# Kernel tuning notes

Hardware: AMD Instinct MI355X
Metric: run time of the kernel (lower is better)

Reference implementation:

```python
import jax, jax.numpy as jnp
import numpy as np

B, N, C, H = 8, 2048, 384, 6
D = C // H  # head dim = 64
SCALE = D ** -0.5


def setup_inputs() -> dict:
    key = jax.random.key(0)
    k1, k2, k3, k4 = jax.random.split(key, 4)
    x = jax.random.normal(k1, (B, N, C), dtype=jnp.float32)
    prompt = jnp.zeros((1,), dtype=jnp.float32)  # unused by forward
    mask = jax.random.uniform(k2, (B, N, N), dtype=jnp.float32)
    qkv_w = jax.random.normal(k3, (3 * C, C), dtype=jnp.float32) * (C ** -0.5)
    proj_w = jax.random.normal(k4, (C, C), dtype=jnp.float32) * (C ** -0.5)
    proj_b = jnp.zeros((C,), dtype=jnp.float32)
    return {"x": x, "prompt": prompt, "mask": mask,
            "qkv_w": qkv_w, "proj_w": proj_w, "proj_b": proj_b}


def reference(x, prompt, mask, qkv_w, proj_w, proj_b):
    b, n, c = x.shape
    # qkv: Linear(dim, 3*dim, bias=False) -> (B,N,3,H,D) -> (3,B,H,N,D)
    qkv = (x @ qkv_w.T).reshape(b, n, 3, H, D).transpose(2, 0, 3, 1, 4)
    q, k, v = qkv[0], qkv[1], qkv[2]
    # attn scores with additive mask (mask * -1e5), softmax over keys
    attn = jnp.einsum('bhqd,bhkd->bhqk', q, k) * SCALE
    attn = attn + (mask * -100000.0)[:, None, :, :]
    attn = jax.nn.softmax(attn, axis=-1)
    out = jnp.einsum('bhqk,bhkd->bhqd', attn, v)  # (B,H,N,D)
    out = out.transpose(0, 2, 1, 3).reshape(b, n, c)
    return out @ proj_w.T + proj_b
```

## Files before the change

### kernel.cpp

```cpp
#include <hip/hip_runtime.h>
#include <stdint.h>
#include <math.h>

#define BB 8
#define SEQ 2048
#define CDIM 384
#define NH 6
#define HD 64
#define QKVN 1152

typedef __attribute__((ext_vector_type(8))) __bf16 bf16x8;
typedef __attribute__((ext_vector_type(4))) __bf16 bf16x4;
typedef __attribute__((ext_vector_type(4))) float f32x4;
typedef __attribute__((ext_vector_type(4))) unsigned short ushort4v;

__device__ __forceinline__ unsigned short f2bf(float f) {
  unsigned int u = __float_as_uint(f);
  u += 0x7fffu + ((u >> 16) & 1u);
  return (unsigned short)(u >> 16);
}

__global__ void k_convert(const float* __restrict__ src, unsigned short* __restrict__ dst, int n4) {
  int i = blockIdx.x * blockDim.x + threadIdx.x;
  if (i >= n4) return;
  float4 f = reinterpret_cast<const float4*>(src)[i];
  ushort4v u;
  u.x = f2bf(f.x); u.y = f2bf(f.y); u.z = f2bf(f.z); u.w = f2bf(f.w);
  reinterpret_cast<ushort4v*>(dst)[i] = u;
}

__device__ __forceinline__ void gload_lds16(const unsigned short* g, unsigned short* l) {
  __builtin_amdgcn_global_load_lds((const __attribute__((address_space(1))) void*)g,
                                   (__attribute__((address_space(3))) void*)l, 16, 0, 0);
}

template<int OUT_F32>
__global__ __launch_bounds__(256, 2) void k_gemm_bt(
    const unsigned short* __restrict__ A, const unsigned short* __restrict__ Bm,
    unsigned short* __restrict__ Cb, float* __restrict__ Cf,
    const float* __restrict__ bias, int M, int Nc, int K)
{
  __shared__ unsigned short lA[128 * 32];
  __shared__ unsigned short lB[128 * 32];
  const int t = threadIdx.x;
  const int w = t >> 6, l = t & 63;
  const int wr = w >> 1, wc = w & 1;
  const int row0 = blockIdx.x * 128, col0 = blockIdx.y * 128;
  const f32x4 vzero = {0.f, 0.f, 0.f, 0.f};
  f32x4 acc[4][4];
#pragma unroll
  for (int m = 0; m < 4; ++m)
#pragma unroll
    for (int n = 0; n < 4; ++n) acc[m][n] = vzero;

  const int srow = w * 16 + (l >> 2);
  const int scol = (l & 3) * 8;
  const int lr = l & 15, kc = (l >> 4) * 8;

  for (int k0 = 0; k0 < K; k0 += 32) {
#pragma unroll
    for (int r = 0; r < 2; ++r) {
      gload_lds16(A + (size_t)(row0 + r * 64 + srow) * K + k0 + scol,
                  &lA[(r * 64 + srow) * 32 + scol]);
      gload_lds16(Bm + (size_t)(col0 + r * 64 + srow) * K + k0 + scol,
                  &lB[(r * 64 + srow) * 32 + scol]);
    }
    __syncthreads();
    bf16x8 af[4], bfr[4];
#pragma unroll
    for (int m = 0; m < 4; ++m)
      af[m] = *(const bf16x8*)&lA[(wr * 64 + m * 16 + lr) * 32 + kc];
#pragma unroll
    for (int n = 0; n < 4; ++n)
      bfr[n] = *(const bf16x8*)&lB[(wc * 64 + n * 16 + lr) * 32 + kc];
#pragma unroll
    for (int m = 0; m < 4; ++m)
#pragma unroll
      for (int n = 0; n < 4; ++n)
        acc[m][n] = __builtin_amdgcn_mfma_f32_16x16x32_bf16(af[m], bfr[n], acc[m][n], 0, 0, 0);
    __syncthreads();
  }

#pragma unroll
  for (int m = 0; m < 4; ++m) {
    const int row = row0 + wr * 64 + m * 16 + (l >> 4) * 4;
#pragma unroll
    for (int n = 0; n < 4; ++n) {
      const int col = col0 + wc * 64 + n * 16 + (l & 15);
      if (OUT_F32) {
        const float bv = bias[col];
#pragma unroll
        for (int j = 0; j < 4; ++j)
          Cf[(size_t)(row + j) * Nc + col] = acc[m][n][j] + bv;
      } else {
#pragma unroll
        for (int j = 0; j < 4; ++j)
          Cb[(size_t)(row + j) * Nc + col] = f2bf(acc[m][n][j]);
      }
    }
  }
}

__global__ void k_vtrans(const unsigned short* __restrict__ qkv, unsigned short* __restrict__ vt)
{
  __shared__ unsigned short tile[64][76];
  const int bh = blockIdx.x;
  const int b = bh / NH, h = bh - b * NH;
  const int n0 = blockIdx.y * 64;
  const int t = threadIdx.x;
  const int rr0 = t >> 4;
  const int c4 = (t & 15) * 4;
  const unsigned short* src = qkv + (size_t)(b * SEQ + n0) * QKVN + 2 * CDIM + h * HD;
#pragma unroll
  for (int rr = 0; rr < 4; ++rr) {
    int n = rr * 16 + rr0;
    ushort4v v = *(const ushort4v*)(src + (size_t)n * QKVN + c4);
    *(ushort4v*)&tile[n][c4] = v;
  }
  __syncthreads();
  unsigned short* dst = vt + (size_t)bh * HD * SEQ + n0;
#pragma unroll
  for (int rr = 0; rr < 4; ++rr) {
    int d = rr * 16 + rr0;
    ushort4v v;
    v.x = tile[c4 + 0][d];
    v.y = tile[c4 + 1][d];
    v.z = tile[c4 + 2][d];
    v.w = tile[c4 + 3][d];
    *(ushort4v*)(dst + (size_t)d * SEQ + c4) = v;
  }
}

__global__ __launch_bounds__(256, 4) void k_attn(
    const unsigned short* __restrict__ qkv, const float* __restrict__ mask,
    const unsigned short* __restrict__ vt, unsigned short* __restrict__ aout)
{
  const int bid = blockIdx.x;
  const int b = bid & 7;
  const int g2 = bid >> 3;
  const int h = g2 % NH;
  const int nt = g2 / NH;
  const int t = threadIdx.x;
  const int w = t >> 6, l = t & 63;
  const int gk = l >> 4, c = l & 15;
  const int q0 = nt * 64 + w * 16;

  __shared__ unsigned short lK[2][4096];
  __shared__ unsigned short lV[2][4096];

  const unsigned short* qb = qkv + (size_t)(b * SEQ + q0) * QKVN + h * HD;
  const unsigned short* kb = qkv + (size_t)(b * SEQ) * QKVN + CDIM + h * HD;
  const unsigned short* vb = vt + (size_t)(b * NH + h) * HD * SEQ;
  const float* mrowc = mask + ((size_t)b * SEQ + q0 + c) * SEQ + 4 * gk;

  const int trow = t >> 3, tg = t & 7;
  const int glog = tg ^ (trow & 7);
  const size_t kSrc = (size_t)trow * QKVN + glog * 8;
  const size_t vSrc = (size_t)trow * SEQ + glog * 8;
  const int tid8 = t * 8;

  const int fr0 = c * 64 + ((gk) ^ (c & 7)) * 8;
  const int fr1 = c * 64 + ((4 + gk) ^ (c & 7)) * 8;
  const int cx2 = 2 * (c & 7);
  const int vg0 = c * 64 + ((gk) ^ cx2) * 4;
  const int vg1 = c * 64 + ((4 + gk) ^ cx2) * 4;
  const int vg2 = c * 64 + ((8 + gk) ^ cx2) * 4;
  const int vg3 = c * 64 + ((12 + gk) ^ cx2) * 4;

  bf16x8 qf0 = *(const bf16x8*)(qb + (size_t)c * QKVN + gk * 8);
  bf16x8 qf1 = *(const bf16x8*)(qb + (size_t)c * QKVN + 32 + gk * 8);
#pragma unroll
  for (int i = 0; i < 8; ++i) {
    qf0[i] = (__bf16)((float)qf0[i] * 0.18033688f);
    qf1[i] = (__bf16)((float)qf1[i] * 0.18033688f);
  }

  const f32x4 vzero = {0.f, 0.f, 0.f, 0.f};
  f32x4 acco[4];
  float mreg = -INFINITY, asum = 0.f;
#pragma unroll
  for (int dt = 0; dt < 4; ++dt) acco[dt] = vzero;

#pragma unroll
  for (int j = 0; j < 2; ++j) {
    gload_lds16(kb + (size_t)j * 32 * QKVN + kSrc, &lK[0][j * 2048 + tid8]);
    gload_lds16(vb + (size_t)j * 32 * SEQ + vSrc, &lV[0][j * 2048 + tid8]);
  }
  float4 mk[4];
#pragma unroll
  for (int j = 0; j < 4; ++j)
    mk[j] = *(const float4*)(mrowc + 16 * j);
  int buf = 0;

  for (int kt = 0; kt < SEQ; kt += 64) {
    const bool haveNext = (kt + 64 < SEQ);
    __syncthreads();
    if (haveNext) {
#pragma unroll
      for (int j = 0; j < 2; ++j) {
        gload_lds16(kb + (size_t)(kt + 64 + j * 32) * QKVN + kSrc, &lK[buf ^ 1][j * 2048 + tid8]);
        gload_lds16(vb + (kt + 64) + (size_t)j * 32 * SEQ + vSrc, &lV[buf ^ 1][j * 2048 + tid8]);
      }
    }

    f32x4 s[4];
#pragma unroll
    for (int j = 0; j < 4; ++j) {
      bf16x8 kfa = *(const bf16x8*)&lK[buf][j * 1024 + fr0];
      bf16x8 kfb = *(const bf16x8*)&lK[buf][j * 1024 + fr1];
      s[j] = __builtin_amdgcn_mfma_f32_16x16x32_bf16(kfa, qf0, vzero, 0, 0, 0);
      s[j] = __builtin_amdgcn_mfma_f32_16x16x32_bf16(kfb, qf1, s[j], 0, 0, 0);
    }

#pragma unroll
    for (int j = 0; j < 4; ++j) {
      const float* mkf = (const float*)&mk[j];
#pragma unroll
      for (int r = 0; r < 4; ++r)
        s[j][r] = fmaf(mkf[r], -144269.50f, s[j][r]);
    }
    if (haveNext) {
#pragma unroll
      for (int j = 0; j < 4; ++j)
        mk[j] = *(const float4*)(mrowc + kt + 64 + 16 * j);
    }

    float tm = fmaxf(fmaxf(fmaxf(s[0][0], s[0][1]), fmaxf(s[0][2], s[0][3])),
                     fmaxf(fmaxf(s[1][0], s[1][1]), fmaxf(s[1][2], s[1][3])));
    tm = fmaxf(tm, fmaxf(fmaxf(fmaxf(s[2][0], s[2][1]), fmaxf(s[2][2], s[2][3])),
                         fmaxf(fmaxf(s[3][0], s[3][1]), fmaxf(s[3][2], s[3][3]))));
    tm = fmaxf(tm, __shfl_xor(tm, 16));
    tm = fmaxf(tm, __shfl_xor(tm, 32));

    if (__any(tm > mreg + 8.f)) {
      const float mn = fmaxf(mreg, tm);
      const float al = __builtin_amdgcn_exp2f(mreg - mn);
      mreg = mn;
      asum *= al;
      float alr[4];
#pragma unroll
      for (int r = 0; r < 4; ++r)
        alr[r] = __shfl(al, 20 * gk + r);
#pragma unroll
      for (int dt = 0; dt < 4; ++dt)
#pragma unroll
        for (int r = 0; r < 4; ++r)
          acco[dt][r] *= alr[r];
    }

#pragma unroll
    for (int j = 0; j < 4; ++j)
#pragma unroll
      for (int r = 0; r < 4; ++r)
        s[j][r] = __builtin_amdgcn_exp2f(s[j][r] - mreg);
    float rs = ((s[0][0] + s[0][1]) + (s[0][2] + s[0][3]))
             + ((s[1][0] + s[1][1]) + (s[1][2] + s[1][3]))
             + ((s[2][0] + s[2][1]) + (s[2][2] + s[2][3]))
             + ((s[3][0] + s[3][1]) + (s[3][2] + s[3][3]));
    rs += __shfl_xor(rs, 16);
    rs += __shfl_xor(rs, 32);
    asum += rs;

    union { unsigned int u[8]; bf16x8 v[2]; } pu;
#pragma unroll
    for (int j = 0; j < 4; ++j) {
      asm("v_cvt_pk_bf16_f32 %0, %1, %2" : "=v"(pu.u[2 * j]) : "v"(s[j][0]), "v"(s[j][1]));
      asm("v_cvt_pk_bf16_f32 %0, %1, %2" : "=v"(pu.u[2 * j + 1]) : "v"(s[j][2]), "v"(s[j][3]));
    }
    bf16x8 pf0 = pu.v[0];
    bf16x8 pf1 = pu.v[1];

#pragma unroll
    for (int dt = 0; dt < 4; ++dt) {
      const unsigned short* vrow = &lV[buf][dt * 1024];
      bf16x4 a0 = *(const bf16x4*)(vrow + vg0);
      bf16x4 a1 = *(const bf16x4*)(vrow + vg1);
      bf16x4 a2 = *(const bf16x4*)(vrow + vg2);
      bf16x4 a3 = *(const bf16x4*)(vrow + vg3);
      bf16x8 vf0 = __builtin_shufflevector(a0, a1, 0, 1, 2, 3, 4, 5, 6, 7);
      bf16x8 vf1 = __builtin_shufflevector(a2, a3, 0, 1, 2, 3, 4, 5, 6, 7);
      acco[dt] = __builtin_amdgcn_mfma_f32_16x16x32_bf16(pf0, vf0, acco[dt], 0, 0, 0);
      acco[dt] = __builtin_amdgcn_mfma_f32_16x16x32_bf16(pf1, vf1, acco[dt], 0, 0, 0);
    }
    buf ^= 1;
  }

  float invr[4];
#pragma unroll
  for (int r = 0; r < 4; ++r)
    invr[r] = 1.0f / __shfl(asum, 20 * gk + r);
  unsigned short* ob = aout + (size_t)(b * SEQ + q0) * CDIM + h * HD;
#pragma unroll
  for (int r = 0; r < 4; ++r)
#pragma unroll
    for (int dt = 0; dt < 4; ++dt)
      ob[(size_t)(4 * gk + r) * CDIM + dt * 16 + c] = f2bf(acco[dt][r] * invr[r]);
}

extern "C" void kernel_launch(void* const* d_in, const int* in_sizes, int n_in,
                              void* d_out, int out_size, void* d_ws, size_t ws_size,
                              hipStream_t stream) {
  (void)in_sizes; (void)n_in; (void)out_size; (void)ws_size;
  const float* x      = (const float*)d_in[0];
  const float* mask   = (const float*)d_in[2];
  const float* qkv_w  = (const float*)d_in[3];
  const float* proj_w = (const float*)d_in[4];
  const float* proj_b = (const float*)d_in[5];
  float* out = (float*)d_out;
  char* ws = (char*)d_ws;

  unsigned short* xb    = (unsigned short*)(ws + 0);
  unsigned short* wqb   = (unsigned short*)(ws + 12582912);
  unsigned short* wpb   = (unsigned short*)(ws + 13467648);
  unsigned short* qkvb  = (unsigned short*)(ws + 13762560);
  unsigned short* vtb   = (unsigned short*)(ws + 51511296);
  unsigned short* aoutb = (unsigned short*)(ws + 64094208);

  k_convert<<<6144, 256, 0, stream>>>(x, xb, 1572864);
  k_convert<<<432, 256, 0, stream>>>(qkv_w, wqb, 110592);
  k_convert<<<144, 256, 0, stream>>>(proj_w, wpb, 36864);
  k_gemm_bt<0><<<dim3(128, 9), 256, 0, stream>>>(xb, wqb, qkvb, nullptr, nullptr, 16384, 1152, 384);
  k_vtrans<<<dim3(48, 32), 256, 0, stream>>>(qkvb, vtb);
  k_attn<<<1536, 256, 0, stream>>>(qkvb, mask, vtb, aoutb);
  k_gemm_bt<1><<<dim3(128, 3), 256, 0, stream>>>(aoutb, wpb, nullptr, out, proj_b, 16384, 384, 384);
}
```

Measured before the change: 198.2 us.

## Rework attention kernel to 32x32 MFMA tiles with 32 queries per wave

The attention kernel now has each wave handle 32 query rows using 32x32x16 bf16 MFMAs instead of 16 rows with 16x16x32 MFMAs. This doubles the queries per block, halves the grid, and lets each K/V tile loaded into LDS serve twice as many queries. The softmax row sum is now computed by an extra MFMA against a ones vector, and P is rearranged with permlane32 swaps. It also adds s_setprio around the MFMA sections and loads the mask inside the loop instead of prefetching it. The cost is higher register pressure (launch bounds lowered to 2) and less latency hiding on the mask loads.

```diff
diff --git a/kernel.cpp b/kernel.cpp
--- a/kernel.cpp
+++ b/kernel.cpp
@@ -10,8 +10,8 @@
 #define QKVN 1152
 
 typedef __attribute__((ext_vector_type(8))) __bf16 bf16x8;
-typedef __attribute__((ext_vector_type(4))) __bf16 bf16x4;
 typedef __attribute__((ext_vector_type(4))) float f32x4;
+typedef __attribute__((ext_vector_type(16))) float f32x16;
 typedef __attribute__((ext_vector_type(4))) unsigned short ushort4v;
 
 __device__ __forceinline__ unsigned short f2bf(float f) {
@@ -131,7 +131,7 @@
   }
 }
 
-__global__ __launch_bounds__(256, 4) void k_attn(
+__global__ __launch_bounds__(256, 2) void k_attn(
     const unsigned short* __restrict__ qkv, const float* __restrict__ mask,
     const unsigned short* __restrict__ vt, unsigned short* __restrict__ aout)
 {
@@ -142,16 +142,15 @@
   const int nt = g2 / NH;
   const int t = threadIdx.x;
   const int w = t >> 6, l = t & 63;
-  const int gk = l >> 4, c = l & 15;
-  const int q0 = nt * 64 + w * 16;
+  const int ql = l & 31, hl = l >> 5;
+  const int q0w = nt * 128 + w * 32;
 
   __shared__ unsigned short lK[2][4096];
   __shared__ unsigned short lV[2][4096];
 
-  const unsigned short* qb = qkv + (size_t)(b * SEQ + q0) * QKVN + h * HD;
   const unsigned short* kb = qkv + (size_t)(b * SEQ) * QKVN + CDIM + h * HD;
   const unsigned short* vb = vt + (size_t)(b * NH + h) * HD * SEQ;
-  const float* mrowc = mask + ((size_t)b * SEQ + q0 + c) * SEQ + 4 * gk;
+  const float* mrowq = mask + ((size_t)b * SEQ + q0w + ql) * SEQ + 4 * hl;
 
   const int trow = t >> 3, tg = t & 7;
   const int glog = tg ^ (trow & 7);
@@ -159,37 +158,37 @@
   const size_t vSrc = (size_t)trow * SEQ + glog * 8;
   const int tid8 = t * 8;
 
-  const int fr0 = c * 64 + ((gk) ^ (c & 7)) * 8;
-  const int fr1 = c * 64 + ((4 + gk) ^ (c & 7)) * 8;
-  const int cx2 = 2 * (c & 7);
-  const int vg0 = c * 64 + ((gk) ^ cx2) * 4;
-  const int vg1 = c * 64 + ((4 + gk) ^ cx2) * 4;
-  const int vg2 = c * 64 + ((8 + gk) ^ cx2) * 4;
-  const int vg3 = c * 64 + ((12 + gk) ^ cx2) * 4;
-
-  bf16x8 qf0 = *(const bf16x8*)(qb + (size_t)c * QKVN + gk * 8);
-  bf16x8 qf1 = *(const bf16x8*)(qb + (size_t)c * QKVN + 32 + gk * 8);
-#pragma unroll
-  for (int i = 0; i < 8; ++i) {
-    qf0[i] = (__bf16)((float)qf0[i] * 0.18033688f);
-    qf1[i] = (__bf16)((float)qf1[i] * 0.18033688f);
-  }
-
-  const f32x4 vzero = {0.f, 0.f, 0.f, 0.f};
-  f32x4 acco[4];
-  float mreg = -INFINITY, asum = 0.f;
-#pragma unroll
-  for (int dt = 0; dt < 4; ++dt) acco[dt] = vzero;
+  const int qx = ql & 7;
+  int off0[4], off1[4];
+#pragma unroll
+  for (int i = 0; i < 4; ++i) {
+    const int g = ((2 * i + hl) ^ qx) * 8;
+    off0[i] = ql * 64 + g;
+    off1[i] = (32 + ql) * 64 + g;
+  }
+
+  const unsigned short* qb = qkv + (size_t)(b * SEQ + q0w + ql) * QKVN + h * HD;
+  bf16x8 qf[4];
+#pragma unroll
+  for (int m = 0; m < 4; ++m) {
+    qf[m] = *(const bf16x8*)(qb + 16 * m + 8 * hl);
+#pragma unroll
+    for (int i = 0; i < 8; ++i)
+      qf[m][i] = (__bf16)((float)qf[m][i] * 0.18033688f);
+  }
+
+  const __bf16 one = (__bf16)1.0f;
+  const bf16x8 vones = {one, one, one, one, one, one, one, one};
+  f32x16 acco0, acco1, asum;
+#pragma unroll
+  for (int i = 0; i < 16; ++i) { acco0[i] = 0.f; acco1[i] = 0.f; asum[i] = 0.f; }
+  float mreg = -INFINITY;
 
 #pragma unroll
   for (int j = 0; j < 2; ++j) {
     gload_lds16(kb + (size_t)j * 32 * QKVN + kSrc, &lK[0][j * 2048 + tid8]);
     gload_lds16(vb + (size_t)j * 32 * SEQ + vSrc, &lV[0][j * 2048 + tid8]);
   }
-  float4 mk[4];
-#pragma unroll
-  for (int j = 0; j < 4; ++j)
-    mk[j] = *(const float4*)(mrowc + 16 * j);
   int buf = 0;
 
   for (int kt = 0; kt < SEQ; kt += 64) {
@@ -203,98 +202,101 @@
       }
     }
 
-    f32x4 s[4];
+    float4 mk[8];
+#pragma unroll
+    for (int s = 0; s < 8; ++s)
+      mk[s] = *(const float4*)(mrowq + kt + 8 * s);
+
+    f32x16 s0, s1;
+#pragma unroll
+    for (int i = 0; i < 16; ++i) { s0[i] = 0.f; s1[i] = 0.f; }
+    __builtin_amdgcn_s_setprio(1);
+#pragma unroll
+    for (int m = 0; m < 4; ++m) {
+      bf16x8 kfa = *(const bf16x8*)&lK[buf][off0[m]];
+      bf16x8 kfb = *(const bf16x8*)&lK[buf][off1[m]];
+      s0 = __builtin_amdgcn_mfma_f32_32x32x16_bf16(kfa, qf[m], s0, 0, 0, 0);
+      s1 = __builtin_amdgcn_mfma_f32_32x32x16_bf16(kfb, qf[m], s1, 0, 0, 0);
+    }
+    __builtin_amdgcn_s_setprio(0);
+
 #pragma unroll
     for (int j = 0; j < 4; ++j) {
-      bf16x8 kfa = *(const bf16x8*)&lK[buf][j * 1024 + fr0];
-      bf16x8 kfb = *(const bf16x8*)&lK[buf][j * 1024 + fr1];
-      s[j] = __builtin_amdgcn_mfma_f32_16x16x32_bf16(kfa, qf0, vzero, 0, 0, 0);
-      s[j] = __builtin_amdgcn_mfma_f32_16x16x32_bf16(kfb, qf1, s[j], 0, 0, 0);
-    }
-
-#pragma unroll
-    for (int j = 0; j < 4; ++j) {
-      const float* mkf = (const float*)&mk[j];
-#pragma unroll
-      for (int r = 0; r < 4; ++r)
-        s[j][r] = fmaf(mkf[r], -144269.50f, s[j][r]);
-    }
-    if (haveNext) {
-#pragma unroll
-      for (int j = 0; j < 4; ++j)
-        mk[j] = *(const float4*)(mrowc + kt + 64 + 16 * j);
-    }
-
-    float tm = fmaxf(fmaxf(fmaxf(s[0][0], s[0][1]), fmaxf(s[0][2], s[0][3])),
-                     fmaxf(fmaxf(s[1][0], s[1][1]), fmaxf(s[1][2], s[1][3])));
-    tm = fmaxf(tm, fmaxf(fmaxf(fmaxf(s[2][0], s[2][1]), fmaxf(s[2][2], s[2][3])),
-                         fmaxf(fmaxf(s[3][0], s[3][1]), fmaxf(s[3][2], s[3][3]))));
-    tm = fmaxf(tm, __shfl_xor(tm, 16));
+      const float* m0 = (const float*)&mk[j];
+      const float* m1 = (const float*)&mk[4 + j];
+#pragma unroll
+      for (int r = 0; r < 4; ++r) {
+        s0[4 * j + r] = fmaf(m0[r], -144269.50f, s0[4 * j + r]);
+        s1[4 * j + r] = fmaf(m1[r], -144269.50f, s1[4 * j + r]);
+      }
+    }
+
+    float tm = fmaxf(fmaxf(s0[0], s0[1]), fmaxf(s0[2], s0[3]));
+#pragma unroll
+    for (int i = 4; i < 16; i += 4)
+      tm = fmaxf(tm, fmaxf(fmaxf(s0[i], s0[i + 1]), fmaxf(s0[i + 2], s0[i + 3])));
+#pragma unroll
+    for (int i = 0; i < 16; i += 4)
+      tm = fmaxf(tm, fmaxf(fmaxf(s1[i], s1[i + 1]), fmaxf(s1[i + 2], s1[i + 3])));
     tm = fmaxf(tm, __shfl_xor(tm, 32));
 
     if (__any(tm > mreg + 8.f)) {
       const float mn = fmaxf(mreg, tm);
       const float al = __builtin_amdgcn_exp2f(mreg - mn);
       mreg = mn;
-      asum *= al;
-      float alr[4];
-#pragma unroll
-      for (int r = 0; r < 4; ++r)
-        alr[r] = __shfl(al, 20 * gk + r);
-#pragma unroll
-      for (int dt = 0; dt < 4; ++dt)
-#pragma unroll
-        for (int r = 0; r < 4; ++r)
-          acco[dt][r] *= alr[r];
-    }
-
-#pragma unroll
-    for (int j = 0; j < 4; ++j)
-#pragma unroll
-      for (int r = 0; r < 4; ++r)
-        s[j][r] = __builtin_amdgcn_exp2f(s[j][r] - mreg);
-    float rs = ((s[0][0] + s[0][1]) + (s[0][2] + s[0][3]))
-             + ((s[1][0] + s[1][1]) + (s[1][2] + s[1][3]))
-             + ((s[2][0] + s[2][1]) + (s[2][2] + s[2][3]))
-             + ((s[3][0] + s[3][1]) + (s[3][2] + s[3][3]));
-    rs += __shfl_xor(rs, 16);
-    rs += __shfl_xor(rs, 32);
-    asum += rs;
-
-    union { unsigned int u[8]; bf16x8 v[2]; } pu;
+#pragma unroll
+      for (int reg = 0; reg < 16; ++reg) {
+        const float alr = __shfl(al, (reg & 3) + 8 * (reg >> 2) + 4 * hl);
+        asum[reg] *= alr;
+        acco0[reg] *= alr;
+        acco1[reg] *= alr;
+      }
+    }
+
+#pragma unroll
+    for (int i = 0; i < 16; ++i) {
+      s0[i] = __builtin_amdgcn_exp2f(s0[i] - mreg);
+      s1[i] = __builtin_amdgcn_exp2f(s1[i] - mreg);
+    }
+
+    unsigned pk0[8], pk1[8];
 #pragma unroll
     for (int j = 0; j < 4; ++j) {
-      asm("v_cvt_pk_bf16_f32 %0, %1, %2" : "=v"(pu.u[2 * j]) : "v"(s[j][0]), "v"(s[j][1]));
-      asm("v_cvt_pk_bf16_f32 %0, %1, %2" : "=v"(pu.u[2 * j + 1]) : "v"(s[j][2]), "v"(s[j][3]));
-    }
-    bf16x8 pf0 = pu.v[0];
-    bf16x8 pf1 = pu.v[1];
-
-#pragma unroll
-    for (int dt = 0; dt < 4; ++dt) {
-      const unsigned short* vrow = &lV[buf][dt * 1024];
-      bf16x4 a0 = *(const bf16x4*)(vrow + vg0);
-      bf16x4 a1 = *(const bf16x4*)(vrow + vg1);
-      bf16x4 a2 = *(const bf16x4*)(vrow + vg2);
-      bf16x4 a3 = *(const bf16x4*)(vrow + vg3);
-      bf16x8 vf0 = __builtin_shufflevector(a0, a1, 0, 1, 2, 3, 4, 5, 6, 7);
-      bf16x8 vf1 = __builtin_shufflevector(a2, a3, 0, 1, 2, 3, 4, 5, 6, 7);
-      acco[dt] = __builtin_amdgcn_mfma_f32_16x16x32_bf16(pf0, vf0, acco[dt], 0, 0, 0);
-      acco[dt] = __builtin_amdgcn_mfma_f32_16x16x32_bf16(pf1, vf1, acco[dt], 0, 0, 0);
-    }
+      asm("v_cvt_pk_bf16_f32 %0, %1, %2" : "=v"(pk0[2 * j]) : "v"(s0[4 * j]), "v"(s0[4 * j + 1]));
+      asm("v_cvt_pk_bf16_f32 %0, %1, %2" : "=v"(pk0[2 * j + 1]) : "v"(s0[4 * j + 2]), "v"(s0[4 * j + 3]));
+      asm("v_cvt_pk_bf16_f32 %0, %1, %2" : "=v"(pk1[2 * j]) : "v"(s1[4 * j]), "v"(s1[4 * j + 1]));
+      asm("v_cvt_pk_bf16_f32 %0, %1, %2" : "=v"(pk1[2 * j + 1]) : "v"(s1[4 * j + 2]), "v"(s1[4 * j + 3]));
+    }
+
+    __builtin_amdgcn_s_setprio(1);
+#pragma unroll
+    for (int kc = 0; kc < 4; ++kc) {
+      const unsigned* pkb = (kc < 2) ? pk0 : pk1;
+      const int base = 4 * (kc & 1);
+      unsigned x0 = pkb[base + 0], y0 = pkb[base + 2];
+      unsigned x1 = pkb[base + 1], y1 = pkb[base + 3];
+      asm("v_permlane32_swap_b32 %0, %1" : "+v"(x0), "+v"(y0));
+      asm("v_permlane32_swap_b32 %0, %1" : "+v"(x1), "+v"(y1));
+      union { unsigned u[4]; bf16x8 v; } A;
+      A.u[0] = x0; A.u[1] = x1; A.u[2] = y0; A.u[3] = y1;
+      asum = __builtin_amdgcn_mfma_f32_32x32x16_bf16(A.v, vones, asum, 0, 0, 0);
+      bf16x8 vf0 = *(const bf16x8*)&lV[buf][off0[kc]];
+      bf16x8 vf1 = *(const bf16x8*)&lV[buf][off1[kc]];
+      acco0 = __builtin_amdgcn_mfma_f32_32x32x16_bf16(A.v, vf0, acco0, 0, 0, 0);
+      acco1 = __builtin_amdgcn_mfma_f32_32x32x16_bf16(A.v, vf1, acco1, 0, 0, 0);
+    }
+    __builtin_amdgcn_s_setprio(0);
     buf ^= 1;
   }
 
-  float invr[4];
-#pragma unroll
-  for (int r = 0; r < 4; ++r)
-    invr[r] = 1.0f / __shfl(asum, 20 * gk + r);
-  unsigned short* ob = aout + (size_t)(b * SEQ + q0) * CDIM + h * HD;
-#pragma unroll
-  for (int r = 0; r < 4; ++r)
-#pragma unroll
-    for (int dt = 0; dt < 4; ++dt)
-      ob[(size_t)(4 * gk + r) * CDIM + dt * 16 + c] = f2bf(acco[dt][r] * invr[r]);
+  unsigned short* ob = aout + (size_t)(b * SEQ + q0w) * CDIM + h * HD;
+#pragma unroll
+  for (int reg = 0; reg < 16; ++reg) {
+    const float inv = 1.0f / asum[reg];
+    const int qrow = (reg & 3) + 8 * (reg >> 2) + 4 * hl;
+    ob[(size_t)qrow * CDIM + ql] = f2bf(acco0[reg] * inv);
+    ob[(size_t)qrow * CDIM + 32 + ql] = f2bf(acco1[reg] * inv);
+  }
 }
 
 extern "C" void kernel_launch(void* const* d_in, const int* in_sizes, int n_in,
@@ -321,6 +323,6 @@
   k_convert<<<144, 256, 0, stream>>>(proj_w, wpb, 36864);
   k_gemm_bt<0><<<dim3(128, 9), 256, 0, stream>>>(xb, wqb, qkvb, nullptr, nullptr, 16384, 1152, 384);
   k_vtrans<<<dim3(48, 32), 256, 0, stream>>>(qkvb, vtb);
-  k_attn<<<1536, 256, 0, stream>>>(qkvb, mask, vtb, aoutb);
+  k_attn<<<768, 256, 0, stream>>>(qkvb, mask, vtb, aoutb);
   k_gemm_bt<1><<<dim3(128, 3), 256, 0, stream>>>(aoutb, wpb, nullptr, out, proj_b, 16384, 384, 384);
 }
```

Result: faster. 178.3 us (-10.1%).
